# Performance work log

Hardware: AMD Instinct MI355X
Metric: run time of the kernel (lower is better)

Reference implementation:

```python
import jax, jax.numpy as jnp
import numpy as np

N_ATOMS = 100_000
N_BONDS = 200_000
MAX_NB = 6
ATOM_FDIM = 133
BOND_FDIM = 147
HIDDEN = 256
DEPTH = 5
ATOMS_PER_MOL = 100


def setup_inputs() -> dict:
    key = jax.random.key(0)
    ks = jax.random.split(key, 9)
    f_atoms = jax.random.normal(ks[0], (N_ATOMS, ATOM_FDIM), dtype=jnp.float32)
    f_bonds = jax.random.normal(ks[1], (N_BONDS, BOND_FDIM), dtype=jnp.float32)
    a2b = jax.random.randint(ks[2], (N_ATOMS, MAX_NB), 0, N_BONDS, dtype=jnp.int32)
    b2a = jax.random.randint(ks[3], (N_BONDS,), 0, N_ATOMS, dtype=jnp.int32)
    # reverse bond of 2i is 2i+1 and vice versa (chemprop directed-bond pairing)
    b2revb = (jnp.arange(N_BONDS, dtype=jnp.int32) ^ 1)
    s_i = 1.0 / np.sqrt(BOND_FDIM)
    s_h = 1.0 / np.sqrt(HIDDEN)
    s_o = 1.0 / np.sqrt(ATOM_FDIM + HIDDEN)
    W_i = jax.random.uniform(ks[4], (HIDDEN, BOND_FDIM), jnp.float32, -s_i, s_i)
    W_h = jax.random.uniform(ks[5], (HIDDEN, HIDDEN), jnp.float32, -s_h, s_h)
    W_o = jax.random.uniform(ks[6], (HIDDEN, ATOM_FDIM + HIDDEN), jnp.float32, -s_o, s_o)
    b_o = jax.random.uniform(ks[7], (HIDDEN,), jnp.float32, -s_o, s_o)
    return {"f_atoms": f_atoms, "f_bonds": f_bonds, "a2b": a2b, "b2a": b2a,
            "b2revb": b2revb, "W_i": W_i, "W_h": W_h, "W_o": W_o, "b_o": b_o,
            "atoms_per_mol": ATOMS_PER_MOL}


def reference(f_atoms, f_bonds, a2b, b2a, b2revb, W_i, W_h, W_o, b_o, atoms_per_mol):
    # input = W_i(f_bonds); message = relu(input)   [n_bonds, H]
    inp = jnp.einsum('bf,hf->bh', f_bonds, W_i)
    message = jax.nn.relu(inp)
    for _ in range(DEPTH - 1):
        # gather incoming-bond messages per atom and sum: [n_atoms, max_nb, H] -> [n_atoms, H]
        a_message = message[a2b].sum(axis=1)
        # directed-MPNN update: subtract reverse-bond message
        m = a_message[b2a] - message[b2revb]
        message = jax.nn.relu(inp + jnp.einsum('bh,gh->bg', m, W_h))
        # dropout p=0.0 (eval) -> identity
    a_message = message[a2b].sum(axis=1)                      # [n_atoms, H]
    a_input = jnp.concatenate([f_atoms, a_message], axis=1)   # [n_atoms, atom_fdim+H]
    atom_hiddens = jax.nn.relu(jnp.einsum('af,hf->ah', a_input, W_o) + b_o)
    # uniform a_scope: stack per-molecule atom blocks -> [n_mols, atoms_per_mol, H]
    return atom_hiddens.reshape(-1, atoms_per_mol, HIDDEN)
```

## Files before the change

kernel.cpp:

```cpp
#include <hip/hip_runtime.h>
#include <hip/hip_bf16.h>

typedef unsigned short u16;
typedef unsigned short u16x8 __attribute__((ext_vector_type(8)));
typedef short s8vec __attribute__((ext_vector_type(8)));
typedef float f4vec __attribute__((ext_vector_type(4)));

__device__ __forceinline__ float bf2f(u16 u) {
    union { unsigned int i; float f; } c; c.i = ((unsigned int)u) << 16; return c.f;
}
__device__ __forceinline__ u16 f2bf(float f) {
    union { float f; unsigned int i; } c; c.f = f;
    unsigned int x = c.i;
    x += 0x7fffu + ((x >> 16) & 1u);
    return (u16)(x >> 16);
}
__device__ __forceinline__ void gload_lds16(const void* g, void* l) {
    __builtin_amdgcn_global_load_lds((__attribute__((address_space(1))) void*)g,
                                     (__attribute__((address_space(3))) void*)l, 16, 0, 0);
}

__global__ void pad_w_all(const float* __restrict__ W_i, const float* __restrict__ W_h,
                          const float* __restrict__ W_o,
                          u16* __restrict__ Wi, u16* __restrict__ Wh,
                          u16* __restrict__ Wo2, u16* __restrict__ Wo1) {
    int r = blockIdx.x;
    int which = blockIdx.y;
    const float* src; u16* dst; int sstride, col0, nvalid, dcol;
    if (which == 0)      { src = W_i; dst = Wi;  sstride = 147; col0 = 0;   nvalid = 147; dcol = 192; }
    else if (which == 1) { src = W_h; dst = Wh;  sstride = 256; col0 = 0;   nvalid = 256; dcol = 256; }
    else if (which == 2) { src = W_o; dst = Wo2; sstride = 389; col0 = 133; nvalid = 256; dcol = 256; }
    else                 { src = W_o; dst = Wo1; sstride = 389; col0 = 0;   nvalid = 133; dcol = 192; }
    for (int c = threadIdx.x; c < dcol; c += blockDim.x) {
        float v = (c < nvalid) ? src[(size_t)r * sstride + col0 + c] : 0.f;
        dst[(size_t)r * dcol + c] = f2bf(v);
    }
}

__global__ void gather6_kernel(const u16* __restrict__ P, const int* __restrict__ a2b,
                               u16* __restrict__ out, int n_atoms) {
    int lane = threadIdx.x & 63;
    int half = lane >> 5;
    int col = (lane & 31) * 8;
    int wid = (blockIdx.x * blockDim.x + threadIdx.x) >> 6;
    int nw = (gridDim.x * blockDim.x) >> 6;
    for (int a0 = wid * 2; a0 < n_atoms; a0 += nw * 2) {
        int a = a0 + half;
        float acc[8];
#pragma unroll
        for (int e = 0; e < 8; ++e) acc[e] = 0.f;
#pragma unroll
        for (int j = 0; j < 6; ++j) {
            int b = a2b[a * 6 + j];
            u16x8 v = *(const u16x8*)(P + (size_t)b * 256 + col);
#pragma unroll
            for (int e = 0; e < 8; ++e) acc[e] += bf2f(v[e]);
        }
        u16x8 o;
#pragma unroll
        for (int e = 0; e < 8; ++e) o[e] = f2bf(acc[e]);
        *(u16x8*)(out + (size_t)a * 256 + col) = o;
    }
}

template <int ASTAGE, int EPI, int KP>
__launch_bounds__(1024, 4)
__global__ void gemm_smem(const void* __restrict__ Asrc, const u16* __restrict__ Pm,
                          const u16* __restrict__ aPm, const int* __restrict__ b2a,
                          const u16* __restrict__ Bw, int M, int scol,
                          void* __restrict__ out0, const u16* __restrict__ aQ,
                          const float* __restrict__ bias) {
    constexpr int CPR = KP / 8;
    constexpr int NKS = KP / 32;
    __shared__ __align__(16) char smem[256 * KP * 2];

    const int t = threadIdx.x;
    const int w = t >> 6, lane = t & 63;
    const int ln15 = lane & 15, hi = lane >> 4;

    constexpr int ITER = (256 * CPR) / 1024;
#pragma unroll
    for (int i = 0; i < ITER; ++i) {
        int d = i * 1024 + t;
        int row = d / CPR, pc = d % CPR;
        int c = pc ^ (row & 7);
        gload_lds16(Bw + (size_t)row * KP + c * 8, &smem[(size_t)(i * 1024 + w * 64) * 16]);
    }
    __syncthreads();

    const int ntiles = M / 16;
    const int cnt = (ntiles + gridDim.x - 1) / gridDim.x;
    const int t0 = blockIdx.x * cnt;

    for (int it = w; it < cnt; it += 16) {
        const int tile = t0 + it;
        if (tile >= ntiles) break;
        const int r0 = tile * 16;
        const int gr = r0 + ln15;

        int nb = 0;
        if (ASTAGE == 4) nb = b2a[gr];
        u16x8 a[NKS];
#pragma unroll
        for (int ks = 0; ks < NKS; ++ks) {
            const int coff = ks * 32 + hi * 8;
            u16x8 v;
            if (ASTAGE == 1) {
                const float* src = (const float*)Asrc + (size_t)gr * scol;
#pragma unroll
                for (int e = 0; e < 8; ++e) {
                    float x = 0.f;
                    if (coff + e < scol) x = src[coff + e];
                    v[e] = f2bf(x);
                }
            } else if (ASTAGE == 2) {
                u16x8 x = *(const u16x8*)((const u16*)Asrc + (size_t)gr * 256 + coff);
#pragma unroll
                for (int e = 0; e < 8; ++e) v[e] = (x[e] >> 15) ? (u16)0 : x[e];
            } else {
                u16x8 vi = *(const u16x8*)((const u16*)Asrc + (size_t)gr * 256 + coff);
                u16x8 vp = *(const u16x8*)(Pm + (size_t)(gr ^ 1) * 256 + coff);
                u16x8 va = *(const u16x8*)(aPm + (size_t)nb * 256 + coff);
#pragma unroll
                for (int e = 0; e < 8; ++e)
                    v[e] = f2bf(fmaxf(bf2f(vi[e]) + bf2f(va[e]) - bf2f(vp[e]), 0.f));
            }
            a[ks] = v;
        }

        f4vec acc[16];
#pragma unroll
        for (int j = 0; j < 16; ++j) acc[j] = (f4vec){0.f, 0.f, 0.f, 0.f};
#pragma unroll
        for (int ks = 0; ks < NKS; ++ks) {
#pragma unroll
            for (int j = 0; j < 16; ++j) {
                const int rowc = j * 16 + ln15;
                const int phys = (ks * 4 + hi) ^ (rowc & 7);
                s8vec bf = *(const s8vec*)&smem[rowc * (CPR * 16) + phys * 16];
                acc[j] = __builtin_amdgcn_mfma_f32_16x16x32_bf16(
                    *(const s8vec*)&a[ks], bf, acc[j], 0, 0, 0);
            }
        }

#pragma unroll
        for (int j = 0; j < 16; ++j) {
            const int C = j * 16 + ln15;
#pragma unroll
            for (int r = 0; r < 4; ++r) {
                const int R = r0 + hi * 4 + r;
                float vv = acc[j][r];
                if (EPI == 0) {
                    ((u16*)out0)[(size_t)R * 256 + C] = f2bf(vv);
                } else {
                    float o = vv + bf2f(aQ[(size_t)R * 256 + C]) + bias[C];
                    ((float*)out0)[(size_t)R * 256 + C] = fmaxf(o, 0.f);
                }
            }
        }
    }
}

extern "C" void kernel_launch(void* const* d_in, const int* in_sizes, int n_in,
                              void* d_out, int out_size, void* d_ws, size_t ws_size,
                              hipStream_t stream) {
    const float* f_atoms = (const float*)d_in[0];
    const float* f_bonds = (const float*)d_in[1];
    const int* a2b = (const int*)d_in[2];
    const int* b2a = (const int*)d_in[3];
    const float* W_i = (const float*)d_in[5];
    const float* W_h = (const float*)d_in[6];
    const float* W_o = (const float*)d_in[7];
    const float* b_o = (const float*)d_in[8];

    const int NA = 100000, NB = 200000;

    char* ws = (char*)d_ws;
    u16* inp = (u16*)(ws + 0);
    u16* Pa  = (u16*)(ws + 102400000);
    u16* Pb  = (u16*)(ws + 204800000);
    u16* aP  = (u16*)(ws + 307200000);
    u16* Wi  = (u16*)(ws + 358400000);
    u16* Wh  = (u16*)(ws + 358498304);
    u16* Wo2 = (u16*)(ws + 358629376);
    u16* Wo1 = (u16*)(ws + 358760448);
    if (ws_size < 358858752u) return;

    pad_w_all<<<dim3(256, 4), dim3(256), 0, stream>>>(W_i, W_h, W_o, Wi, Wh, Wo2, Wo1);

    gemm_smem<1, 0, 192><<<dim3(256), dim3(1024), 0, stream>>>(
        f_bonds, nullptr, nullptr, nullptr, Wi, NB, 147, inp, nullptr, nullptr);

    gemm_smem<2, 0, 256><<<dim3(256), dim3(1024), 0, stream>>>(
        inp, nullptr, nullptr, nullptr, Wh, NB, 0, Pa, nullptr, nullptr);
    gather6_kernel<<<dim3(2048), dim3(256), 0, stream>>>(Pa, a2b, aP, NA);

    u16* Pcur = Pa; u16* Pnxt = Pb;
    for (int it = 0; it < 3; ++it) {
        gemm_smem<4, 0, 256><<<dim3(256), dim3(1024), 0, stream>>>(
            inp, Pcur, aP, b2a, Wh, NB, 0, Pnxt, nullptr, nullptr);
        gather6_kernel<<<dim3(2048), dim3(256), 0, stream>>>(Pnxt, a2b, aP, NA);
        u16* tmp = Pcur; Pcur = Pnxt; Pnxt = tmp;
    }

    gemm_smem<4, 0, 256><<<dim3(256), dim3(1024), 0, stream>>>(
        inp, Pcur, aP, b2a, Wo2, NB, 0, Pnxt, nullptr, nullptr);
    gather6_kernel<<<dim3(2048), dim3(256), 0, stream>>>(Pnxt, a2b, aP, NA);

    gemm_smem<1, 3, 192><<<dim3(256), dim3(1024), 0, stream>>>(
        f_atoms, nullptr, nullptr, nullptr, Wo1, NA, 133, d_out, aP, b_o);
}
```

Before: 876.0 us.

## Pre-pad inputs to bf16, fragment-ordered weight LDS, split-K prefetch, 768-thread blocks

Adds a separate pad_rows kernel that converts the fp32 bond and atom feature matrices into padded bf16 buffers, so the GEMMs read vectorized bf16 instead of doing scalar fp32 loads. The weight tile is stored in LDS in MFMA-fragment order, which drops the XOR swizzle address math. The A-operand loads are split in two halves so the second half's global loads are issued before the first half's MFMAs run. Blocks shrink from 1024 to 768 threads, and rounding switches to the HIP bf16 intrinsic. The cost is an extra pass over the input features and more workspace.

```diff
diff --git a/kernel.cpp b/kernel.cpp
--- a/kernel.cpp
+++ b/kernel.cpp
@@ -9,15 +9,31 @@
 __device__ __forceinline__ float bf2f(u16 u) {
     union { unsigned int i; float f; } c; c.i = ((unsigned int)u) << 16; return c.f;
 }
-__device__ __forceinline__ u16 f2bf(float f) {
-    union { float f; unsigned int i; } c; c.f = f;
-    unsigned int x = c.i;
-    x += 0x7fffu + ((x >> 16) & 1u);
-    return (u16)(x >> 16);
+__device__ __forceinline__ u16 f2bfc(float f) {
+    __hip_bfloat16 h = __float2bfloat16(f);
+    return __builtin_bit_cast(u16, h);
 }
 __device__ __forceinline__ void gload_lds16(const void* g, void* l) {
     __builtin_amdgcn_global_load_lds((__attribute__((address_space(1))) void*)g,
                                      (__attribute__((address_space(3))) void*)l, 16, 0, 0);
+}
+
+__global__ void pad_rows(const float* __restrict__ src, u16* __restrict__ dst,
+                         int rows, int scol, int dcol) {
+    size_t total4 = (size_t)rows * dcol / 4;
+    for (size_t i = blockIdx.x * (size_t)blockDim.x + threadIdx.x; i < total4;
+         i += (size_t)gridDim.x * blockDim.x) {
+        size_t idx = i * 4;
+        int r = (int)(idx / dcol);
+        int c = (int)(idx % dcol);
+        const float* s = src + (size_t)r * scol + c;
+        ushort4 o;
+        o.x = (c + 0 < scol) ? f2bfc(s[0]) : (u16)0;
+        o.y = (c + 1 < scol) ? f2bfc(s[1]) : (u16)0;
+        o.z = (c + 2 < scol) ? f2bfc(s[2]) : (u16)0;
+        o.w = (c + 3 < scol) ? f2bfc(s[3]) : (u16)0;
+        *(ushort4*)(dst + idx) = o;
+    }
 }
 
 __global__ void pad_w_all(const float* __restrict__ W_i, const float* __restrict__ W_h,
@@ -33,7 +49,7 @@
     else                 { src = W_o; dst = Wo1; sstride = 389; col0 = 0;   nvalid = 133; dcol = 192; }
     for (int c = threadIdx.x; c < dcol; c += blockDim.x) {
         float v = (c < nvalid) ? src[(size_t)r * sstride + col0 + c] : 0.f;
-        dst[(size_t)r * dcol + c] = f2bf(v);
+        dst[(size_t)r * dcol + c] = f2bfc(v);
     }
 }
 
@@ -58,91 +74,110 @@
         }
         u16x8 o;
 #pragma unroll
-        for (int e = 0; e < 8; ++e) o[e] = f2bf(acc[e]);
+        for (int e = 0; e < 8; ++e) o[e] = f2bfc(acc[e]);
         *(u16x8*)(out + (size_t)a * 256 + col) = o;
     }
 }
 
 template <int ASTAGE, int EPI, int KP>
-__launch_bounds__(1024, 4)
-__global__ void gemm_smem(const void* __restrict__ Asrc, const u16* __restrict__ Pm,
+__launch_bounds__(768, 3)
+__global__ void gemm_smem(const u16* __restrict__ Asrc, const u16* __restrict__ Pm,
                           const u16* __restrict__ aPm, const int* __restrict__ b2a,
-                          const u16* __restrict__ Bw, int M, int scol,
+                          const u16* __restrict__ Bw, int M,
                           void* __restrict__ out0, const u16* __restrict__ aQ,
                           const float* __restrict__ bias) {
-    constexpr int CPR = KP / 8;
     constexpr int NKS = KP / 32;
-    __shared__ __align__(16) char smem[256 * KP * 2];
+    constexpr int NFRAG = NKS * 16;
+    constexpr int H = NKS / 2;
+    __shared__ __align__(16) char smem[NFRAG * 1024];
 
     const int t = threadIdx.x;
     const int w = t >> 6, lane = t & 63;
     const int ln15 = lane & 15, hi = lane >> 4;
 
-    constexpr int ITER = (256 * CPR) / 1024;
-#pragma unroll
-    for (int i = 0; i < ITER; ++i) {
-        int d = i * 1024 + t;
-        int row = d / CPR, pc = d % CPR;
-        int c = pc ^ (row & 7);
-        gload_lds16(Bw + (size_t)row * KP + c * 8, &smem[(size_t)(i * 1024 + w * 64) * 16]);
+    for (int f = w; f < NFRAG; f += 12) {
+        int ks = f >> 4, j = f & 15;
+        const u16* gp = Bw + (size_t)(j * 16 + ln15) * KP + ks * 32 + hi * 8;
+        gload_lds16(gp, &smem[f * 1024]);
     }
     __syncthreads();
 
     const int ntiles = M / 16;
     const int cnt = (ntiles + gridDim.x - 1) / gridDim.x;
-    const int t0 = blockIdx.x * cnt;
-
-    for (int it = w; it < cnt; it += 16) {
-        const int tile = t0 + it;
-        if (tile >= ntiles) break;
-        const int r0 = tile * 16;
-        const int gr = r0 + ln15;
-
-        int nb = 0;
-        if (ASTAGE == 4) nb = b2a[gr];
+    const int tile0 = blockIdx.x * cnt;
+    const int tend = (ntiles - tile0 < cnt) ? (ntiles - tile0) : cnt;
+    const int lbase = lane * 16;
+
+    for (int it = w; it < tend; it += 12) {
+        const int gr = (tile0 + it) * 16 + ln15;
+        const u16* pi = Asrc + (size_t)gr * KP;
+        const u16* pp; const u16* pv;
+        if (ASTAGE == 4) {
+            pp = Pm + (size_t)(gr ^ 1) * KP;
+            pv = aPm + (size_t)b2a[gr] * KP;
+        }
+
         u16x8 a[NKS];
-#pragma unroll
-        for (int ks = 0; ks < NKS; ++ks) {
-            const int coff = ks * 32 + hi * 8;
+        u16x8 p0[3][H], p1[3][H];
+
+#pragma unroll
+        for (int k = 0; k < H; ++k) {
+            const int co = k * 32 + hi * 8;
+            p0[0][k] = *(const u16x8*)(pi + co);
+            if (ASTAGE == 4) { p0[1][k] = *(const u16x8*)(pp + co); p0[2][k] = *(const u16x8*)(pv + co); }
+        }
+#pragma unroll
+        for (int k = 0; k < H; ++k) {
             u16x8 v;
-            if (ASTAGE == 1) {
-                const float* src = (const float*)Asrc + (size_t)gr * scol;
-#pragma unroll
-                for (int e = 0; e < 8; ++e) {
-                    float x = 0.f;
-                    if (coff + e < scol) x = src[coff + e];
-                    v[e] = f2bf(x);
-                }
-            } else if (ASTAGE == 2) {
-                u16x8 x = *(const u16x8*)((const u16*)Asrc + (size_t)gr * 256 + coff);
-#pragma unroll
-                for (int e = 0; e < 8; ++e) v[e] = (x[e] >> 15) ? (u16)0 : x[e];
-            } else {
-                u16x8 vi = *(const u16x8*)((const u16*)Asrc + (size_t)gr * 256 + coff);
-                u16x8 vp = *(const u16x8*)(Pm + (size_t)(gr ^ 1) * 256 + coff);
-                u16x8 va = *(const u16x8*)(aPm + (size_t)nb * 256 + coff);
-#pragma unroll
-                for (int e = 0; e < 8; ++e)
-                    v[e] = f2bf(fmaxf(bf2f(vi[e]) + bf2f(va[e]) - bf2f(vp[e]), 0.f));
-            }
-            a[ks] = v;
+#pragma unroll
+            for (int e = 0; e < 8; ++e) {
+                if (ASTAGE == 0) v[e] = p0[0][k][e];
+                else if (ASTAGE == 2) v[e] = (p0[0][k][e] >> 15) ? (u16)0 : p0[0][k][e];
+                else v[e] = f2bfc(fmaxf(bf2f(p0[0][k][e]) + bf2f(p0[2][k][e]) - bf2f(p0[1][k][e]), 0.f));
+            }
+            a[k] = v;
+        }
+#pragma unroll
+        for (int k = 0; k < H; ++k) {
+            const int co = (H + k) * 32 + hi * 8;
+            p1[0][k] = *(const u16x8*)(pi + co);
+            if (ASTAGE == 4) { p1[1][k] = *(const u16x8*)(pp + co); p1[2][k] = *(const u16x8*)(pv + co); }
         }
 
         f4vec acc[16];
 #pragma unroll
         for (int j = 0; j < 16; ++j) acc[j] = (f4vec){0.f, 0.f, 0.f, 0.f};
-#pragma unroll
-        for (int ks = 0; ks < NKS; ++ks) {
+
+#pragma unroll
+        for (int ks = 0; ks < H; ++ks)
 #pragma unroll
             for (int j = 0; j < 16; ++j) {
-                const int rowc = j * 16 + ln15;
-                const int phys = (ks * 4 + hi) ^ (rowc & 7);
-                s8vec bf = *(const s8vec*)&smem[rowc * (CPR * 16) + phys * 16];
+                s8vec bf = *(const s8vec*)&smem[(ks * 16 + j) * 1024 + lbase];
                 acc[j] = __builtin_amdgcn_mfma_f32_16x16x32_bf16(
                     *(const s8vec*)&a[ks], bf, acc[j], 0, 0, 0);
             }
-        }
-
+
+#pragma unroll
+        for (int k = 0; k < H; ++k) {
+            u16x8 v;
+#pragma unroll
+            for (int e = 0; e < 8; ++e) {
+                if (ASTAGE == 0) v[e] = p1[0][k][e];
+                else if (ASTAGE == 2) v[e] = (p1[0][k][e] >> 15) ? (u16)0 : p1[0][k][e];
+                else v[e] = f2bfc(fmaxf(bf2f(p1[0][k][e]) + bf2f(p1[2][k][e]) - bf2f(p1[1][k][e]), 0.f));
+            }
+            a[H + k] = v;
+        }
+#pragma unroll
+        for (int ks = H; ks < NKS; ++ks)
+#pragma unroll
+            for (int j = 0; j < 16; ++j) {
+                s8vec bf = *(const s8vec*)&smem[(ks * 16 + j) * 1024 + lbase];
+                acc[j] = __builtin_amdgcn_mfma_f32_16x16x32_bf16(
+                    *(const s8vec*)&a[ks], bf, acc[j], 0, 0, 0);
+            }
+
+        const int r0 = (tile0 + it) * 16;
 #pragma unroll
         for (int j = 0; j < 16; ++j) {
             const int C = j * 16 + ln15;
@@ -151,7 +186,7 @@
                 const int R = r0 + hi * 4 + r;
                 float vv = acc[j][r];
                 if (EPI == 0) {
-                    ((u16*)out0)[(size_t)R * 256 + C] = f2bf(vv);
+                    ((u16*)out0)[(size_t)R * 256 + C] = f2bfc(vv);
                 } else {
                     float o = vv + bf2f(aQ[(size_t)R * 256 + C]) + bias[C];
                     ((float*)out0)[(size_t)R * 256 + C] = fmaxf(o, 0.f);
@@ -176,37 +211,42 @@
     const int NA = 100000, NB = 200000;
 
     char* ws = (char*)d_ws;
-    u16* inp = (u16*)(ws + 0);
-    u16* Pa  = (u16*)(ws + 102400000);
-    u16* Pb  = (u16*)(ws + 204800000);
-    u16* aP  = (u16*)(ws + 307200000);
-    u16* Wi  = (u16*)(ws + 358400000);
-    u16* Wh  = (u16*)(ws + 358498304);
-    u16* Wo2 = (u16*)(ws + 358629376);
-    u16* Wo1 = (u16*)(ws + 358760448);
-    if (ws_size < 358858752u) return;
+    u16* fb  = (u16*)(ws + 0);
+    u16* fa  = (u16*)(ws + 0);
+    u16* inp = (u16*)(ws + 76800000);
+    u16* Pa  = (u16*)(ws + 179200000);
+    u16* Pb  = (u16*)(ws + 281600000);
+    u16* aP  = (u16*)(ws + 384000000);
+    u16* Wi  = (u16*)(ws + 435200000);
+    u16* Wh  = (u16*)(ws + 435298304);
+    u16* Wo2 = (u16*)(ws + 435429376);
+    u16* Wo1 = (u16*)(ws + 435560448);
+    if (ws_size < 435658752u) return;
 
     pad_w_all<<<dim3(256, 4), dim3(256), 0, stream>>>(W_i, W_h, W_o, Wi, Wh, Wo2, Wo1);
-
-    gemm_smem<1, 0, 192><<<dim3(256), dim3(1024), 0, stream>>>(
-        f_bonds, nullptr, nullptr, nullptr, Wi, NB, 147, inp, nullptr, nullptr);
-
-    gemm_smem<2, 0, 256><<<dim3(256), dim3(1024), 0, stream>>>(
-        inp, nullptr, nullptr, nullptr, Wh, NB, 0, Pa, nullptr, nullptr);
+    pad_rows<<<dim3(2048), dim3(256), 0, stream>>>(f_bonds, fb, NB, 147, 192);
+
+    gemm_smem<0, 0, 192><<<dim3(256), dim3(768), 0, stream>>>(
+        fb, nullptr, nullptr, nullptr, Wi, NB, inp, nullptr, nullptr);
+
+    gemm_smem<2, 0, 256><<<dim3(256), dim3(768), 0, stream>>>(
+        inp, nullptr, nullptr, nullptr, Wh, NB, Pa, nullptr, nullptr);
     gather6_kernel<<<dim3(2048), dim3(256), 0, stream>>>(Pa, a2b, aP, NA);
 
     u16* Pcur = Pa; u16* Pnxt = Pb;
     for (int it = 0; it < 3; ++it) {
-        gemm_smem<4, 0, 256><<<dim3(256), dim3(1024), 0, stream>>>(
-            inp, Pcur, aP, b2a, Wh, NB, 0, Pnxt, nullptr, nullptr);
+        gemm_smem<4, 0, 256><<<dim3(256), dim3(768), 0, stream>>>(
+            inp, Pcur, aP, b2a, Wh, NB, Pnxt, nullptr, nullptr);
         gather6_kernel<<<dim3(2048), dim3(256), 0, stream>>>(Pnxt, a2b, aP, NA);
         u16* tmp = Pcur; Pcur = Pnxt; Pnxt = tmp;
     }
 
-    gemm_smem<4, 0, 256><<<dim3(256), dim3(1024), 0, stream>>>(
-        inp, Pcur, aP, b2a, Wo2, NB, 0, Pnxt, nullptr, nullptr);
+    gemm_smem<4, 0, 256><<<dim3(256), dim3(768), 0, stream>>>(
+        inp, Pcur, aP, b2a, Wo2, NB, Pnxt, nullptr, nullptr);
     gather6_kernel<<<dim3(2048), dim3(256), 0, stream>>>(Pnxt, a2b, aP, NA);
 
-    gemm_smem<1, 3, 192><<<dim3(256), dim3(1024), 0, stream>>>(
-        f_atoms, nullptr, nullptr, nullptr, Wo1, NA, 133, d_out, aP, b_o);
-}
+    pad_rows<<<dim3(2048), dim3(256), 0, stream>>>(f_atoms, fa, NA, 133, 192);
+
+    gemm_smem<0, 3, 192><<<dim3(256), dim3(768), 0, stream>>>(
+        fa, nullptr, nullptr, nullptr, Wo1, NA, d_out, aP, b_o);
+}
```

Measured after the change: 3.358 ms. +283.4%, slower.

## Use hardware bf16 convert, batch index loads in gather, raise MFMA priority

Applied to the files above, without the earlier changes.

Replaces the manual round-to-nearest bf16 conversion with the HIP intrinsic conversion. In the gather, the six neighbor indices are loaded as int2 pairs and all six rows are issued before a tree-shaped sum. The GEMM kernel gets row pointers computed up front, branch-free masked loads for the fp32 input stage, and s_setprio around the MFMA loop. Each change trims instruction or latency overhead, but the gains are small and somewhat unrelated.

```diff
diff --git a/kernel.cpp b/kernel.cpp
--- a/kernel.cpp
+++ b/kernel.cpp
@@ -9,11 +9,9 @@
 __device__ __forceinline__ float bf2f(u16 u) {
     union { unsigned int i; float f; } c; c.i = ((unsigned int)u) << 16; return c.f;
 }
-__device__ __forceinline__ u16 f2bf(float f) {
-    union { float f; unsigned int i; } c; c.f = f;
-    unsigned int x = c.i;
-    x += 0x7fffu + ((x >> 16) & 1u);
-    return (u16)(x >> 16);
+__device__ __forceinline__ u16 f2bfc(float f) {
+    __hip_bfloat16 h = __float2bfloat16(f);
+    return __builtin_bit_cast(u16, h);
 }
 __device__ __forceinline__ void gload_lds16(const void* g, void* l) {
     __builtin_amdgcn_global_load_lds((__attribute__((address_space(1))) void*)g,
@@ -33,7 +31,7 @@
     else                 { src = W_o; dst = Wo1; sstride = 389; col0 = 0;   nvalid = 133; dcol = 192; }
     for (int c = threadIdx.x; c < dcol; c += blockDim.x) {
         float v = (c < nvalid) ? src[(size_t)r * sstride + col0 + c] : 0.f;
-        dst[(size_t)r * dcol + c] = f2bf(v);
+        dst[(size_t)r * dcol + c] = f2bfc(v);
     }
 }
 
@@ -46,28 +44,31 @@
     int nw = (gridDim.x * blockDim.x) >> 6;
     for (int a0 = wid * 2; a0 < n_atoms; a0 += nw * 2) {
         int a = a0 + half;
-        float acc[8];
-#pragma unroll
-        for (int e = 0; e < 8; ++e) acc[e] = 0.f;
-#pragma unroll
-        for (int j = 0; j < 6; ++j) {
-            int b = a2b[a * 6 + j];
-            u16x8 v = *(const u16x8*)(P + (size_t)b * 256 + col);
-#pragma unroll
-            for (int e = 0; e < 8; ++e) acc[e] += bf2f(v[e]);
-        }
+        const int* idx = a2b + a * 6;
+        int2 i01 = *(const int2*)idx;
+        int2 i23 = *(const int2*)(idx + 2);
+        int2 i45 = *(const int2*)(idx + 4);
+        u16x8 v0 = *(const u16x8*)(P + (size_t)i01.x * 256 + col);
+        u16x8 v1 = *(const u16x8*)(P + (size_t)i01.y * 256 + col);
+        u16x8 v2 = *(const u16x8*)(P + (size_t)i23.x * 256 + col);
+        u16x8 v3 = *(const u16x8*)(P + (size_t)i23.y * 256 + col);
+        u16x8 v4 = *(const u16x8*)(P + (size_t)i45.x * 256 + col);
+        u16x8 v5 = *(const u16x8*)(P + (size_t)i45.y * 256 + col);
         u16x8 o;
 #pragma unroll
-        for (int e = 0; e < 8; ++e) o[e] = f2bf(acc[e]);
+        for (int e = 0; e < 8; ++e)
+            o[e] = f2bfc(((bf2f(v0[e]) + bf2f(v1[e])) + (bf2f(v2[e]) + bf2f(v3[e])))
+                         + (bf2f(v4[e]) + bf2f(v5[e])));
         *(u16x8*)(out + (size_t)a * 256 + col) = o;
     }
 }
 
 template <int ASTAGE, int EPI, int KP>
 __launch_bounds__(1024, 4)
-__global__ void gemm_smem(const void* __restrict__ Asrc, const u16* __restrict__ Pm,
+__global__ void gemm_smem(const u16* __restrict__ Asrc, const float* __restrict__ AsrcF,
+                          int scol, const u16* __restrict__ Pm,
                           const u16* __restrict__ aPm, const int* __restrict__ b2a,
-                          const u16* __restrict__ Bw, int M, int scol,
+                          const u16* __restrict__ Bw, int M,
                           void* __restrict__ out0, const u16* __restrict__ aQ,
                           const float* __restrict__ bias) {
     constexpr int CPR = KP / 8;
@@ -90,47 +91,58 @@
 
     const int ntiles = M / 16;
     const int cnt = (ntiles + gridDim.x - 1) / gridDim.x;
-    const int t0 = blockIdx.x * cnt;
+    const int tile0 = blockIdx.x * cnt;
 
     for (int it = w; it < cnt; it += 16) {
-        const int tile = t0 + it;
+        const int tile = tile0 + it;
         if (tile >= ntiles) break;
         const int r0 = tile * 16;
         const int gr = r0 + ln15;
-
-        int nb = 0;
-        if (ASTAGE == 4) nb = b2a[gr];
+        const u16* pi = (ASTAGE == 1) ? nullptr : Asrc + (size_t)gr * KP;
+        const u16* pp = nullptr; const u16* pv = nullptr;
+        if (ASTAGE == 4) {
+            pp = Pm + (size_t)(gr ^ 1) * KP;
+            pv = aPm + (size_t)b2a[gr] * KP;
+        }
+
         u16x8 a[NKS];
 #pragma unroll
         for (int ks = 0; ks < NKS; ++ks) {
-            const int coff = ks * 32 + hi * 8;
-            u16x8 v;
+            const int co = ks * 32 + hi * 8;
             if (ASTAGE == 1) {
-                const float* src = (const float*)Asrc + (size_t)gr * scol;
+                const size_t fb0 = (size_t)gr * scol + co;
+                u16x8 v;
 #pragma unroll
                 for (int e = 0; e < 8; ++e) {
-                    float x = 0.f;
-                    if (coff + e < scol) x = src[coff + e];
-                    v[e] = f2bf(x);
+                    const bool ok = (co + e) < scol;
+                    float x = AsrcF[ok ? fb0 + e : 0];
+                    v[e] = ok ? f2bfc(x) : (u16)0;
                 }
+                a[ks] = v;
+            } else if (ASTAGE == 0) {
+                a[ks] = *(const u16x8*)(pi + co);
             } else if (ASTAGE == 2) {
-                u16x8 x = *(const u16x8*)((const u16*)Asrc + (size_t)gr * 256 + coff);
-#pragma unroll
-                for (int e = 0; e < 8; ++e) v[e] = (x[e] >> 15) ? (u16)0 : x[e];
+                u16x8 vi = *(const u16x8*)(pi + co);
+                u16x8 v;
+#pragma unroll
+                for (int e = 0; e < 8; ++e) v[e] = (vi[e] >> 15) ? (u16)0 : vi[e];
+                a[ks] = v;
             } else {
-                u16x8 vi = *(const u16x8*)((const u16*)Asrc + (size_t)gr * 256 + coff);
-                u16x8 vp = *(const u16x8*)(Pm + (size_t)(gr ^ 1) * 256 + coff);
-                u16x8 va = *(const u16x8*)(aPm + (size_t)nb * 256 + coff);
+                u16x8 vi = *(const u16x8*)(pi + co);
+                u16x8 vp = *(const u16x8*)(pp + co);
+                u16x8 va = *(const u16x8*)(pv + co);
+                u16x8 v;
 #pragma unroll
                 for (int e = 0; e < 8; ++e)
-                    v[e] = f2bf(fmaxf(bf2f(vi[e]) + bf2f(va[e]) - bf2f(vp[e]), 0.f));
+                    v[e] = f2bfc(fmaxf(bf2f(vi[e]) + bf2f(va[e]) - bf2f(vp[e]), 0.f));
+                a[ks] = v;
             }
-            a[ks] = v;
         }
 
         f4vec acc[16];
 #pragma unroll
         for (int j = 0; j < 16; ++j) acc[j] = (f4vec){0.f, 0.f, 0.f, 0.f};
+        __builtin_amdgcn_s_setprio(1);
 #pragma unroll
         for (int ks = 0; ks < NKS; ++ks) {
 #pragma unroll
@@ -142,6 +154,7 @@
                     *(const s8vec*)&a[ks], bf, acc[j], 0, 0, 0);
             }
         }
+        __builtin_amdgcn_s_setprio(0);
 
 #pragma unroll
         for (int j = 0; j < 16; ++j) {
@@ -151,7 +164,7 @@
                 const int R = r0 + hi * 4 + r;
                 float vv = acc[j][r];
                 if (EPI == 0) {
-                    ((u16*)out0)[(size_t)R * 256 + C] = f2bf(vv);
+                    ((u16*)out0)[(size_t)R * 256 + C] = f2bfc(vv);
                 } else {
                     float o = vv + bf2f(aQ[(size_t)R * 256 + C]) + bias[C];
                     ((float*)out0)[(size_t)R * 256 + C] = fmaxf(o, 0.f);
@@ -189,24 +202,24 @@
     pad_w_all<<<dim3(256, 4), dim3(256), 0, stream>>>(W_i, W_h, W_o, Wi, Wh, Wo2, Wo1);
 
     gemm_smem<1, 0, 192><<<dim3(256), dim3(1024), 0, stream>>>(
-        f_bonds, nullptr, nullptr, nullptr, Wi, NB, 147, inp, nullptr, nullptr);
+        nullptr, f_bonds, 147, nullptr, nullptr, nullptr, Wi, NB, inp, nullptr, nullptr);
 
     gemm_smem<2, 0, 256><<<dim3(256), dim3(1024), 0, stream>>>(
-        inp, nullptr, nullptr, nullptr, Wh, NB, 0, Pa, nullptr, nullptr);
+        inp, nullptr, 0, nullptr, nullptr, nullptr, Wh, NB, Pa, nullptr, nullptr);
     gather6_kernel<<<dim3(2048), dim3(256), 0, stream>>>(Pa, a2b, aP, NA);
 
     u16* Pcur = Pa; u16* Pnxt = Pb;
     for (int it = 0; it < 3; ++it) {
         gemm_smem<4, 0, 256><<<dim3(256), dim3(1024), 0, stream>>>(
-            inp, Pcur, aP, b2a, Wh, NB, 0, Pnxt, nullptr, nullptr);
+            inp, nullptr, 0, Pcur, aP, b2a, Wh, NB, Pnxt, nullptr, nullptr);
         gather6_kernel<<<dim3(2048), dim3(256), 0, stream>>>(Pnxt, a2b, aP, NA);
         u16* tmp = Pcur; Pcur = Pnxt; Pnxt = tmp;
     }
 
     gemm_smem<4, 0, 256><<<dim3(256), dim3(1024), 0, stream>>>(
-        inp, Pcur, aP, b2a, Wo2, NB, 0, Pnxt, nullptr, nullptr);
+        inp, nullptr, 0, Pcur, aP, b2a, Wo2, NB, Pnxt, nullptr, nullptr);
     gather6_kernel<<<dim3(2048), dim3(256), 0, stream>>>(Pnxt, a2b, aP, NA);
 
     gemm_smem<1, 3, 192><<<dim3(256), dim3(1024), 0, stream>>>(
-        f_atoms, nullptr, nullptr, nullptr, Wo1, NA, 133, d_out, aP, b_o);
-}
+        nullptr, f_atoms, 133, nullptr, nullptr, nullptr, Wo1, NA, d_out, aP, b_o);
+}
```

Result: slower. 945.9 us (+8.0%).
